# Kernel tuning notes

Hardware: AMD Instinct MI355X
Metric: run time of the kernel (lower is better)

## Reference

```python
import jax, jax.numpy as jnp
import numpy as np
import math

N_EMBD = 512
N_HEAD = 8
B, T = 2, 4096


def setup_inputs() -> dict:
    key = jax.random.key(0)
    ks = jax.random.split(key, 12)
    s = 1.0 / math.sqrt(N_EMBD)
    inp = {
        "x": jax.random.normal(ks[0], (B, T, N_EMBD), dtype=jnp.float32),
        "weight": jax.random.uniform(ks[1], (1,), dtype=jnp.float32),
        "state": jax.random.uniform(ks[2], (1,), dtype=jnp.float32),
        "Wq": jax.random.normal(ks[3], (N_EMBD, N_EMBD), dtype=jnp.float32) * s,
        "bq": jnp.zeros((N_EMBD,), dtype=jnp.float32),
        "Wk": jax.random.normal(ks[4], (N_EMBD, N_EMBD), dtype=jnp.float32) * s,
        "bk": jnp.zeros((N_EMBD,), dtype=jnp.float32),
        "Wv": jax.random.normal(ks[5], (N_EMBD, N_EMBD), dtype=jnp.float32) * s,
        "bv": jnp.zeros((N_EMBD,), dtype=jnp.float32),
        "Wp": jax.random.normal(ks[6], (N_EMBD, N_EMBD), dtype=jnp.float32) * s,
        "bp": jnp.zeros((N_EMBD,), dtype=jnp.float32),
    }
    return inp


def reference(x, weight, state, Wq, bq, Wk, bk, Wv, bv, Wp, bp):
    # weight / state are accepted but unused, matching the torch module.
    Bb, Tt, C = x.shape
    hd = C // N_HEAD

    def split_heads(t):  # [B,T,C] -> [B,H,T,hd]
        return t.reshape(Bb, Tt, N_HEAD, hd).transpose(0, 2, 1, 3)

    # torch nn.Linear: y = x @ W.T + b
    q = split_heads(x @ Wq.T + bq)
    k = split_heads(x @ Wk.T + bk)
    v = split_heads(x @ Wv.T + bv)

    scale = 1.0 / math.sqrt(hd)
    att = jnp.einsum("bhqd,bhkd->bhqk", q, k) * scale  # [B,H,T,T]
    causal = jnp.tril(jnp.ones((Tt, Tt), dtype=bool))
    att = jnp.where(causal[None, None, :, :], att, -jnp.inf)
    att = jax.nn.softmax(att, axis=-1)
    # attn_drop / resid_drop are identity (p=0 / eval)
    y = jnp.einsum("bhqk,bhkd->bhqd", att, v)  # [B,H,T,hd]
    y = y.transpose(0, 2, 1, 3).reshape(Bb, Tt, C)
    return y @ Wp.T + bp
```

## Files before the change

### kernel.cpp

```cpp
#include <hip/hip_runtime.h>
#include <math.h>

using short8  = __attribute__((ext_vector_type(8))) short;
using floatx4 = __attribute__((ext_vector_type(4))) float;

#define DEVI __device__ __forceinline__

#define BATCH 2
#define SEQ   4096
#define NE    512
#define NH    8
#define HD    64
#define MTOT  8192

#define QSCALE 0.18033688011112042f

DEVI short f2bf(float f) {
    unsigned u = __builtin_bit_cast(unsigned, f);
    unsigned r = (u + 0x7fffu + ((u >> 16) & 1u)) >> 16;
    return (short)r;
}

DEVI void async16(const void* g, void* l) {
    __builtin_amdgcn_global_load_lds(
        (const __attribute__((address_space(1))) void*)g,
        (__attribute__((address_space(3))) void*)l, 16, 0, 0);
}

__global__ __launch_bounds__(256) void cvt_bf16(const float* __restrict__ src,
                                                short* __restrict__ dst, int n4) {
    int i = blockIdx.x * 256 + threadIdx.x;
    if (i >= n4) return;
    float4 f = ((const float4*)src)[i];
    short4 o;
    o.x = f2bf(f.x); o.y = f2bf(f.y); o.z = f2bf(f.z); o.w = f2bf(f.w);
    ((short4*)dst)[i] = o;
}

DEVI void gemm_mainloop(const short* __restrict__ A, const short* __restrict__ W,
                        int m0, int n0, short* ldsA, short* ldsW, floatx4 (&acc)[4][4]) {
    const int tid  = threadIdx.x;
    const int lane = tid & 63;
    const int w    = tid >> 6;
    const int wm   = w >> 1, wn = w & 1;
    const int quad = lane >> 4, l15 = lane & 15;
    const int srow = lane >> 3, scol = (lane & 7) * 8;

    for (int i = 0; i < 4; ++i)
        for (int j = 0; j < 4; ++j)
            acc[i][j] = floatx4{0.f, 0.f, 0.f, 0.f};

    for (int kt = 0; kt < NE / 64; ++kt) {
        const int k0 = kt * 64;
        for (int c = 0; c < 4; ++c) {
            const int rb = w * 32 + c * 8;
            async16(A + (size_t)(m0 + rb + srow) * NE + k0 + scol, ldsA + rb * 64);
            async16(W + (size_t)(n0 + rb + srow) * NE + k0 + scol, ldsW + rb * 64);
        }
        __syncthreads();
        for (int ks = 0; ks < 2; ++ks) {
            short8 af[4], bf[4];
            for (int i = 0; i < 4; ++i)
                af[i] = *(const short8*)(ldsA + (wm * 64 + i * 16 + l15) * 64 + ks * 32 + quad * 8);
            for (int j = 0; j < 4; ++j)
                bf[j] = *(const short8*)(ldsW + (wn * 64 + j * 16 + l15) * 64 + ks * 32 + quad * 8);
            for (int i = 0; i < 4; ++i)
                for (int j = 0; j < 4; ++j)
                    acc[i][j] = __builtin_amdgcn_mfma_f32_16x16x32_bf16(af[i], bf[j], acc[i][j], 0, 0, 0);
        }
        __syncthreads();
    }
}

__global__ __launch_bounds__(256) void gemm_qkv(const short* __restrict__ xbf,
                                                const short* __restrict__ wbf,
                                                const float* __restrict__ bq,
                                                const float* __restrict__ bk,
                                                const float* __restrict__ bv,
                                                short* __restrict__ qkv) {
    __shared__ short ldsA[128 * 64];
    __shared__ short ldsW[128 * 64];
    const int m0 = blockIdx.x * 128, n0 = blockIdx.y * 128, z = blockIdx.z;
    const short* W = wbf + (size_t)z * (NE * NE);
    const float* bias = (z == 0) ? bq : (z == 1) ? bk : bv;
    short* out = qkv + (size_t)z * (MTOT * NE);

    floatx4 acc[4][4];
    gemm_mainloop(xbf, W, m0, n0, ldsA, ldsW, acc);

    const int lane = threadIdx.x & 63, w = threadIdx.x >> 6;
    const int wm = w >> 1, wn = w & 1, quad = lane >> 4, l15 = lane & 15;
    const float scale = (z == 0) ? QSCALE : 1.0f;
    for (int j = 0; j < 4; ++j) {
        const int col = n0 + wn * 64 + j * 16 + l15;
        const float bz = bias[col];
        const int h = col >> 6, d = col & 63;
        for (int i = 0; i < 4; ++i) {
            for (int r = 0; r < 4; ++r) {
                const int row = m0 + wm * 64 + i * 16 + quad * 4 + r;
                const int b = row >> 12, t = row & 4095;
                const float v = (acc[i][j][r] + bz) * scale;
                if (z == 2) {
                    out[((size_t)(b * NH + h) * HD + d) * SEQ + t] = f2bf(v);
                } else {
                    out[(((size_t)(b * NH + h)) * SEQ + t) * HD + d] = f2bf(v);
                }
            }
        }
    }
}

__global__ __launch_bounds__(256) void gemm_proj(const short* __restrict__ ybf,
                                                 const short* __restrict__ wp,
                                                 const float* __restrict__ bp,
                                                 float* __restrict__ out) {
    __shared__ short ldsA[128 * 64];
    __shared__ short ldsW[128 * 64];
    const int m0 = blockIdx.x * 128, n0 = blockIdx.y * 128;

    floatx4 acc[4][4];
    gemm_mainloop(ybf, wp, m0, n0, ldsA, ldsW, acc);

    const int lane = threadIdx.x & 63, w = threadIdx.x >> 6;
    const int wm = w >> 1, wn = w & 1, quad = lane >> 4, l15 = lane & 15;
    for (int j = 0; j < 4; ++j) {
        const int col = n0 + wn * 64 + j * 16 + l15;
        const float bz = bp[col];
        for (int i = 0; i < 4; ++i) {
            for (int r = 0; r < 4; ++r) {
                const int row = m0 + wm * 64 + i * 16 + quad * 4 + r;
                out[(size_t)row * NE + col] = acc[i][j][r] + bz;
            }
        }
    }
}

__global__ __launch_bounds__(256, 2) void attn(const short* __restrict__ q,
                                               const short* __restrict__ k,
                                               const short* __restrict__ vt,
                                               short* __restrict__ y) {
    const int bx = blockIdx.x;
    const int bh = blockIdx.y;
    const int tid = threadIdx.x, lane = tid & 63, w = tid >> 6;
    const int quad = lane >> 4, l15 = lane & 15;

    __shared__ short ldsK[2][64 * 64];
    __shared__ short ldsV[2][64 * 64];
    __shared__ short ldsP[4][16 * 72];

    const short* K  = k  + (size_t)bh * (SEQ * HD);
    const short* VT = vt + (size_t)bh * (HD * SEQ);
    short* myP = (short*)ldsP[w];
    const int b = bh >> 3, h = bh & 7;

    const int lb   = ((lane & 7) - (lane >> 3)) & 7;
    const int jrow = lane >> 3;
    const int p0 = (quad + (l15 & 7)) & 7;
    const int p1 = p0 ^ 4;

    for (int sel = 0; sel < 2; ++sel) {
        const int qt = sel ? (SEQ / 64 - 1 - bx) : bx;
        const short* Q = q + (size_t)bh * (SEQ * HD) + (size_t)qt * 64 * HD;

        short8 qfrag[2];
#pragma unroll
        for (int ks = 0; ks < 2; ++ks)
            qfrag[ks] = *(const short8*)&Q[(w * 16 + l15) * HD + ks * 32 + quad * 8];

        floatx4 O[4];
        float lsum[4];
#pragma unroll
        for (int n = 0; n < 4; ++n) O[n] = floatx4{0.f, 0.f, 0.f, 0.f};
#pragma unroll
        for (int r = 0; r < 4; ++r) lsum[r] = 0.f;

        __syncthreads();
#pragma unroll
        for (int c2 = 0; c2 < 2; ++c2) {
            const int chunk = w * 2 + c2;
            const int j = chunk * 8 + jrow;
            async16(K + (size_t)j * HD + lb * 8, ldsK[0] + chunk * 512);
            async16(VT + (size_t)j * SEQ + lb * 8, ldsV[0] + chunk * 512);
        }

        for (int jt = 0; jt <= qt; ++jt) {
            __syncthreads();
            const int cur = jt & 1;

            if (jt < qt) {
                const int nx = cur ^ 1;
                const short* Kt = K + (size_t)(jt + 1) * 64 * HD;
                const short* Vc = VT + (jt + 1) * 64;
#pragma unroll
                for (int c2 = 0; c2 < 2; ++c2) {
                    const int chunk = w * 2 + c2;
                    const int j = chunk * 8 + jrow;
                    async16(Kt + (size_t)j * HD + lb * 8, ldsK[nx] + chunk * 512);
                    async16(Vc + (size_t)j * SEQ + lb * 8, ldsV[nx] + chunk * 512);
                }
            }

            const short* bK = ldsK[cur];
            const short* bV = ldsV[cur];
            short8 kf[2][4], vf[2][4];
#pragma unroll
            for (int n = 0; n < 4; ++n) {
                const int row = n * 16 + l15;
                kf[0][n] = *(const short8*)(bK + row * 64 + p0 * 8);
                kf[1][n] = *(const short8*)(bK + row * 64 + p1 * 8);
                vf[0][n] = *(const short8*)(bV + row * 64 + p0 * 8);
                vf[1][n] = *(const short8*)(bV + row * 64 + p1 * 8);
            }

            floatx4 S[4];
#pragma unroll
            for (int n = 0; n < 4; ++n) S[n] = floatx4{0.f, 0.f, 0.f, 0.f};
#pragma unroll
            for (int ks = 0; ks < 2; ++ks)
#pragma unroll
                for (int n = 0; n < 4; ++n)
                    S[n] = __builtin_amdgcn_mfma_f32_16x16x32_bf16(qfrag[ks], kf[ks][n], S[n], 0, 0, 0);

            if (jt == qt) {
#pragma unroll
                for (int n = 0; n < 4; ++n)
#pragma unroll
                    for (int r = 0; r < 4; ++r) {
                        const int rowl = w * 16 + quad * 4 + r;
                        const int coll = n * 16 + l15;
                        if (coll > rowl) S[n][r] = -3.0e38f;
                    }
            }

#pragma unroll
            for (int n = 0; n < 4; ++n)
#pragma unroll
                for (int r = 0; r < 4; ++r)
                    S[n][r] = __builtin_amdgcn_exp2f(S[n][r]);
#pragma unroll
            for (int r = 0; r < 4; ++r)
                lsum[r] += (S[0][r] + S[1][r]) + (S[2][r] + S[3][r]);

#pragma unroll
            for (int n = 0; n < 4; ++n)
#pragma unroll
                for (int r = 0; r < 4; ++r)
                    myP[(quad * 4 + r) * 72 + n * 16 + l15] = f2bf(S[n][r]);

            short8 pf[2];
#pragma unroll
            for (int ks = 0; ks < 2; ++ks)
                pf[ks] = *(const short8*)(myP + l15 * 72 + ks * 32 + quad * 8);

#pragma unroll
            for (int ks = 0; ks < 2; ++ks)
#pragma unroll
                for (int n = 0; n < 4; ++n)
                    O[n] = __builtin_amdgcn_mfma_f32_16x16x32_bf16(pf[ks], vf[ks][n], O[n], 0, 0, 0);
        }

#pragma unroll
        for (int r = 0; r < 4; ++r) {
#pragma unroll
            for (int off = 1; off < 16; off <<= 1)
                lsum[r] += __shfl_xor(lsum[r], off, 64);
        }

#pragma unroll
        for (int r = 0; r < 4; ++r) {
            const float inv = 1.0f / lsum[r];
            const int t = qt * 64 + w * 16 + quad * 4 + r;
#pragma unroll
            for (int n = 0; n < 4; ++n) {
                const int col = h * 64 + n * 16 + l15;
                y[((size_t)(b * SEQ + t)) * NE + col] = f2bf(O[n][r] * inv);
            }
        }
    }
}

extern "C" void kernel_launch(void* const* d_in, const int* in_sizes, int n_in,
                              void* d_out, int out_size, void* d_ws, size_t ws_size,
                              hipStream_t stream) {
    const float* x  = (const float*)d_in[0];
    const float* Wq = (const float*)d_in[3];
    const float* bq = (const float*)d_in[4];
    const float* Wk = (const float*)d_in[5];
    const float* bk = (const float*)d_in[6];
    const float* Wv = (const float*)d_in[7];
    const float* bv = (const float*)d_in[8];
    const float* Wp = (const float*)d_in[9];
    const float* bp = (const float*)d_in[10];
    float* out = (float*)d_out;

    short* ws   = (short*)d_ws;
    short* xbf  = ws;
    short* wbf  = xbf + (size_t)MTOT * NE;
    short* qb   = wbf + 4 * (size_t)NE * NE;
    short* kb   = qb + (size_t)MTOT * NE;
    short* vtb  = kb + (size_t)MTOT * NE;
    short* yb   = vtb + (size_t)MTOT * NE;

    cvt_bf16<<<(MTOT * NE / 4 + 255) / 256, 256, 0, stream>>>(x, xbf, MTOT * NE / 4);
    cvt_bf16<<<(NE * NE / 4 + 255) / 256, 256, 0, stream>>>(Wq, wbf + 0 * (size_t)NE * NE, NE * NE / 4);
    cvt_bf16<<<(NE * NE / 4 + 255) / 256, 256, 0, stream>>>(Wk, wbf + 1 * (size_t)NE * NE, NE * NE / 4);
    cvt_bf16<<<(NE * NE / 4 + 255) / 256, 256, 0, stream>>>(Wv, wbf + 2 * (size_t)NE * NE, NE * NE / 4);
    cvt_bf16<<<(NE * NE / 4 + 255) / 256, 256, 0, stream>>>(Wp, wbf + 3 * (size_t)NE * NE, NE * NE / 4);

    gemm_qkv<<<dim3(MTOT / 128, NE / 128, 3), 256, 0, stream>>>(xbf, wbf, bq, bk, bv, qb);

    attn<<<dim3(SEQ / 128, BATCH * NH), 256, 0, stream>>>(qb, kb, vtb, yb);

    gemm_proj<<<dim3(MTOT / 128, NE / 128), 256, 0, stream>>>(yb, wbf + 3 * (size_t)NE * NE, bp, out);
}
```

Before: 225.9 us.

## Write V row-major, transpose in separate kernel, remap attention block order

The QKV GEMM epilogue now writes V in the same row-major head layout as Q and K, which removes the strided transposed stores that scattered writes along the sequence dimension. A new LDS-tiled transpose kernel builds the V^T layout that attention expects. It reuses the x bf16 buffer as its destination, and the attention output reuses the V buffer. The attention grid is flattened to 1D and the block index is remapped to interleave heads, likely for better scheduling or cache locality. The cost is an extra kernel launch plus an extra read and write pass over V.

Result: faster. 211.9 us (-6.2%).

```diff
diff --git a/kernel.cpp b/kernel.cpp
--- a/kernel.cpp
+++ b/kernel.cpp
@@ -100,13 +100,41 @@
                 const int row = m0 + wm * 64 + i * 16 + quad * 4 + r;
                 const int b = row >> 12, t = row & 4095;
                 const float v = (acc[i][j][r] + bz) * scale;
-                if (z == 2) {
-                    out[((size_t)(b * NH + h) * HD + d) * SEQ + t] = f2bf(v);
-                } else {
-                    out[(((size_t)(b * NH + h)) * SEQ + t) * HD + d] = f2bf(v);
-                }
-            }
-        }
+                out[(((size_t)(b * NH + h)) * SEQ + t) * HD + d] = f2bf(v);
+            }
+        }
+    }
+}
+
+__global__ __launch_bounds__(256) void transpose_v(const short* __restrict__ vb,
+                                                   short* __restrict__ vt) {
+    const int bh = blockIdx.y;
+    const int t0 = blockIdx.x * 64;
+    __shared__ short tile[64 * 66];
+    const int tid = threadIdx.x;
+    const int r  = tid >> 3;
+    const int c8 = tid & 7;
+
+    const short* src = vb + ((size_t)bh * SEQ + t0) * HD;
+#pragma unroll
+    for (int p = 0; p < 2; ++p) {
+        const int row = p * 32 + r;
+        short8 v = *(const short8*)&src[row * HD + c8 * 8];
+#pragma unroll
+        for (int i = 0; i < 8; ++i)
+            tile[row * 66 + c8 * 8 + i] = v[i];
+    }
+    __syncthreads();
+
+    short* dst = vt + (size_t)bh * (HD * SEQ) + t0;
+#pragma unroll
+    for (int p = 0; p < 2; ++p) {
+        const int d = p * 32 + r;
+        short8 o;
+#pragma unroll
+        for (int i = 0; i < 8; ++i)
+            o[i] = tile[(c8 * 8 + i) * 66 + d];
+        *(short8*)&dst[(size_t)d * SEQ + c8 * 8] = o;
     }
 }
 
@@ -139,8 +167,9 @@
                                                const short* __restrict__ k,
                                                const short* __restrict__ vt,
                                                short* __restrict__ y) {
-    const int bx = blockIdx.x;
-    const int bh = blockIdx.y;
+    const int id = blockIdx.x;
+    const int bx = id >> 4;
+    const int bh = ((id & 7) << 1) | ((id >> 3) & 1);
     const int tid = threadIdx.x, lane = tid & 63, w = tid >> 6;
     const int quad = lane >> 4, l15 = lane & 15;
 
@@ -298,8 +327,9 @@
     short* wbf  = xbf + (size_t)MTOT * NE;
     short* qb   = wbf + 4 * (size_t)NE * NE;
     short* kb   = qb + (size_t)MTOT * NE;
-    short* vtb  = kb + (size_t)MTOT * NE;
-    short* yb   = vtb + (size_t)MTOT * NE;
+    short* vb   = kb + (size_t)MTOT * NE;
+    short* vtb  = xbf;
+    short* yb   = vb;
 
     cvt_bf16<<<(MTOT * NE / 4 + 255) / 256, 256, 0, stream>>>(x, xbf, MTOT * NE / 4);
     cvt_bf16<<<(NE * NE / 4 + 255) / 256, 256, 0, stream>>>(Wq, wbf + 0 * (size_t)NE * NE, NE * NE / 4);
@@ -309,7 +339,9 @@
 
     gemm_qkv<<<dim3(MTOT / 128, NE / 128, 3), 256, 0, stream>>>(xbf, wbf, bq, bk, bv, qb);
 
-    attn<<<dim3(SEQ / 128, BATCH * NH), 256, 0, stream>>>(qb, kb, vtb, yb);
+    transpose_v<<<dim3(SEQ / 64, BATCH * NH), 256, 0, stream>>>(vb, vtb);
+
+    attn<<<dim3(512), 256, 0, stream>>>(qb, kb, vtb, yb);
 
     gemm_proj<<<dim3(MTOT / 128, NE / 128), 256, 0, stream>>>(yb, wbf + 3 * (size_t)NE * NE, bp, out);
 }
```
